# Optimization experiments

Hardware: AMD Instinct MI355X
Metric: run time of the kernel (lower is better)

Reference implementation:

```python
import jax, jax.numpy as jnp
import numpy as np

N_NODES = 4096
IN_FEAT = 256
N_HEADS = 8
N_HIDDEN = 64  # out_features // n_heads
NEG_SLOPE = 0.2
EDGE_PROB = 0.05


def setup_inputs() -> dict:
    key = jax.random.key(0)
    k1, k2, k3, k4 = jax.random.split(key, 4)
    h = jax.random.normal(k1, (N_NODES, IN_FEAT), dtype=jnp.float32)
    # binary adjacency mask [N, N, 1] (broadcast over heads), as in the torch asserts
    adj_mat = (jax.random.uniform(k2, (N_NODES, N_NODES, 1)) < EDGE_PROB).astype(jnp.float32)
    # nn.Linear(in_features, n_heads*n_hidden, bias=False) weight: [H*F, in]
    W = jax.random.normal(k3, (N_HEADS * N_HIDDEN, IN_FEAT), dtype=jnp.float32) / np.sqrt(IN_FEAT)
    # nn.Linear(2*n_hidden, 1, bias=False) weight, flattened: [2*F]
    a = jax.random.normal(k4, (2 * N_HIDDEN,), dtype=jnp.float32) / np.sqrt(2 * N_HIDDEN)
    return {"h": h, "adj_mat": adj_mat, "W": W, "a": a}


def reference(h, adj_mat, W, a):
    n = h.shape[0]
    # g: [N, H, F]
    g = (h @ W.T).reshape(n, N_HEADS, N_HIDDEN)
    # attn(cat[g_i, g_j]) == a_l . g_i + a_r . g_j  (linear, no bias)
    a_l = a[:N_HIDDEN]
    a_r = a[N_HIDDEN:]
    el = jnp.einsum('ihf,f->ih', g, a_l)  # [N, H]
    er = jnp.einsum('jhf,f->jh', g, a_r)  # [N, H]
    e = jax.nn.leaky_relu(el[:, None, :] + er[None, :, :], NEG_SLOPE)  # [N, N, H]
    # note: original multiplies scores by adjacency (not masked_fill)
    e = e * adj_mat  # adj broadcasts over heads
    att = jax.nn.softmax(e, axis=1)  # softmax over source nodes j
    # dropout is identity at eval (dropout_rate=0.0)
    out = jnp.einsum('ijh,jhf->ihf', att, g)  # [N, H, F]
    return out.reshape(n, N_HEADS * N_HIDDEN)
```

## Files before the change

kernel.cpp:

```cpp
#include <hip/hip_runtime.h>
#include <float.h>

#define N_NODES 4096
#define IN_FEAT 256
#define N_HEADS 8
#define N_HIDDEN 64
#define OUT_FEAT (N_HEADS * N_HIDDEN)
#define MAXE 512
#define NEG_SLOPE 0.2f

typedef _Float16 half8 __attribute__((ext_vector_type(8)));
typedef float floatx4 __attribute__((ext_vector_type(4)));
typedef float float8v __attribute__((ext_vector_type(8)));

__device__ inline unsigned fkey(float f) {
  unsigned u = __float_as_uint(f);
  return (u & 0x80000000u) ? ~u : (u | 0x80000000u);
}
__device__ inline float fkey_inv(unsigned k) {
  unsigned u = (k & 0x80000000u) ? (k & 0x7fffffffu) : ~k;
  return __uint_as_float(u);
}

__global__ __launch_bounds__(256) void gemm_fused(
    const float* __restrict__ H, const float* __restrict__ Wt,
    const float* __restrict__ a,
    _Float16* __restrict__ G16, float* __restrict__ el, float* __restrict__ er,
    float* __restrict__ gsum, unsigned* __restrict__ ermax_keys) {
  __shared__ _Float16 Ah[64][72], Al[64][72];
  __shared__ _Float16 Bh[64][72], Bl[64][72];
  const int t = threadIdx.x;
  const int w = t >> 6, l = t & 63;
  const int n16 = l & 15, q = l >> 4;
  const int bi = blockIdx.x, bo = blockIdx.y;
  const int m0 = bi * 64 + w * 16;

  floatx4 acc[4];
#pragma unroll
  for (int ct = 0; ct < 4; ++ct) acc[ct] = (floatx4)0.f;

  for (int kc = 0; kc < 4; ++kc) {
    if (kc) __syncthreads();
#pragma unroll
    for (int p = 0; p < 4; ++p) {
      const int idx = p * 256 + t;
      const int r = idx >> 4;
      const int c4 = (idx & 15) * 4;
      float4 hv = *(const float4*)(H + (size_t)(bi * 64 + r) * IN_FEAT + kc * 64 + c4);
      float4 wv = *(const float4*)(Wt + (size_t)(bo * 64 + r) * IN_FEAT + kc * 64 + c4);
      union { _Float16 h[4]; int2 d; } hh_, hl_, wh_, wl_;
      hh_.h[0] = (_Float16)hv.x; hh_.h[1] = (_Float16)hv.y;
      hh_.h[2] = (_Float16)hv.z; hh_.h[3] = (_Float16)hv.w;
      hl_.h[0] = (_Float16)(hv.x - (float)hh_.h[0]);
      hl_.h[1] = (_Float16)(hv.y - (float)hh_.h[1]);
      hl_.h[2] = (_Float16)(hv.z - (float)hh_.h[2]);
      hl_.h[3] = (_Float16)(hv.w - (float)hh_.h[3]);
      wh_.h[0] = (_Float16)wv.x; wh_.h[1] = (_Float16)wv.y;
      wh_.h[2] = (_Float16)wv.z; wh_.h[3] = (_Float16)wv.w;
      wl_.h[0] = (_Float16)(wv.x - (float)wh_.h[0]);
      wl_.h[1] = (_Float16)(wv.y - (float)wh_.h[1]);
      wl_.h[2] = (_Float16)(wv.z - (float)wh_.h[2]);
      wl_.h[3] = (_Float16)(wv.w - (float)wh_.h[3]);
      *(int2*)&Ah[r][c4] = hh_.d;
      *(int2*)&Al[r][c4] = hl_.d;
      *(int2*)&Bh[r][c4] = wh_.d;
      *(int2*)&Bl[r][c4] = wl_.d;
    }
    __syncthreads();
#pragma unroll
    for (int ks = 0; ks < 2; ++ks) {
      half8 Afh = *(const half8*)&Ah[w * 16 + n16][ks * 32 + q * 8];
      half8 Afl = *(const half8*)&Al[w * 16 + n16][ks * 32 + q * 8];
#pragma unroll
      for (int ct = 0; ct < 4; ++ct) {
        half8 Bfh = *(const half8*)&Bh[ct * 16 + n16][ks * 32 + q * 8];
        half8 Bfl = *(const half8*)&Bl[ct * 16 + n16][ks * 32 + q * 8];
        acc[ct] = __builtin_amdgcn_mfma_f32_16x16x32_f16(Afh, Bfh, acc[ct], 0, 0, 0);
        acc[ct] = __builtin_amdgcn_mfma_f32_16x16x32_f16(Afl, Bfh, acc[ct], 0, 0, 0);
        acc[ct] = __builtin_amdgcn_mfma_f32_16x16x32_f16(Afh, Bfl, acc[ct], 0, 0, 0);
      }
    }
  }

  float aLv[4], aRv[4];
#pragma unroll
  for (int ct = 0; ct < 4; ++ct) {
    aLv[ct] = a[ct * 16 + n16];
    aRv[ct] = a[64 + ct * 16 + n16];
  }

  float erv[4];
#pragma unroll
  for (int reg = 0; reg < 4; ++reg) {
    float sl = 0.f, sr = 0.f;
#pragma unroll
    for (int ct = 0; ct < 4; ++ct) {
      sl = fmaf(acc[ct][reg], aLv[ct], sl);
      sr = fmaf(acc[ct][reg], aRv[ct], sr);
    }
#pragma unroll
    for (int off = 1; off < 16; off <<= 1) {
      sl += __shfl_xor(sl, off);
      sr += __shfl_xor(sr, off);
    }
    erv[reg] = sr;
    if (n16 == 0) {
      const int rowi = m0 + q * 4 + reg;
      el[(size_t)rowi * N_HEADS + bo] = sl;
      er[(size_t)rowi * N_HEADS + bo] = sr;
    }
  }

  {
    float mx = fmaxf(fmaxf(erv[0], erv[1]), fmaxf(erv[2], erv[3]));
    mx = fmaxf(mx, __shfl_xor(mx, 16));
    mx = fmaxf(mx, __shfl_xor(mx, 32));
    if (l == 0) atomicMax(ermax_keys + bo, fkey(mx));
  }

#pragma unroll
  for (int ct = 0; ct < 4; ++ct) {
    float s = acc[ct][0] + acc[ct][1] + acc[ct][2] + acc[ct][3];
    s += __shfl_xor(s, 16);
    s += __shfl_xor(s, 32);
    if (l < 16) atomicAdd(gsum + bo * 64 + ct * 16 + n16, s);
  }

#pragma unroll
  for (int ct = 0; ct < 4; ++ct)
#pragma unroll
    for (int reg = 0; reg < 4; ++reg)
      G16[(size_t)(m0 + q * 4 + reg) * OUT_FEAT + bo * 64 + ct * 16 + n16] =
          (_Float16)acc[ct][reg];
}

__global__ __launch_bounds__(256, 8) void attn_sparse(
    const float* __restrict__ adj, const _Float16* __restrict__ G16,
    const float* __restrict__ el, const float* __restrict__ er,
    const unsigned* __restrict__ ermax_keys, const float* __restrict__ gsum,
    float* __restrict__ out) {
  __shared__ int jlist[MAXE];
  __shared__ _Float16 w16[MAXE * N_HEADS];
  __shared__ float accp[4][OUT_FEAT];
  __shared__ float el_s[N_HEADS], ermax_s[N_HEADS];
  __shared__ float zw[4][N_HEADS];
  __shared__ float em_s[N_HEADS], invz_s[N_HEADS];
  __shared__ int cnt;

  const int i = blockIdx.x;
  const int t = threadIdx.x;
  if (t == 0) cnt = 0;
  if (t < N_HEADS) {
    el_s[t] = el[(size_t)i * N_HEADS + t];
    ermax_s[t] = fkey_inv(ermax_keys[t]);
  }
  __syncthreads();

  const float* row = adj + (size_t)i * N_NODES;
#pragma unroll
  for (int q = 0; q < 4; ++q) {
    int j0 = (q * 256 + t) * 4;
    float4 v = *(const float4*)(row + j0);
    if (v.x != 0.f) { int p = atomicAdd(&cnt, 1); if (p < MAXE) jlist[p] = j0; }
    if (v.y != 0.f) { int p = atomicAdd(&cnt, 1); if (p < MAXE) jlist[p] = j0 + 1; }
    if (v.z != 0.f) { int p = atomicAdd(&cnt, 1); if (p < MAXE) jlist[p] = j0 + 2; }
    if (v.w != 0.f) { int p = atomicAdd(&cnt, 1); if (p < MAXE) jlist[p] = j0 + 3; }
  }
  __syncthreads();
  const int deg = min(cnt, MAXE);

  const int h2 = t & 7;
  const float m_h = fmaxf(0.f, el_s[h2] + ermax_s[h2]);
  const float em_h = __expf(-m_h);
  float zacc = 0.f;
  for (int jj = t >> 3; jj < deg; jj += 32) {
    int j = jlist[jj];
    float x = el_s[h2] + er[(size_t)j * N_HEADS + h2];
    x = fmaxf(x, NEG_SLOPE * x);
    float wv = __expf(x - m_h);
    zacc += wv;
    w16[jj * N_HEADS + h2] = (_Float16)wv;
  }
#pragma unroll
  for (int off = 8; off < 64; off <<= 1) zacc += __shfl_xor(zacc, off);
  if ((t & 63) < 8) zw[t >> 6][t & 7] = zacc;
  __syncthreads();
  if (t < 8) {
    float Z = zw[0][t] + zw[1][t] + zw[2][t] + zw[3][t] +
              (float)(N_NODES - deg) * em_h;
    invz_s[t] = 1.f / Z;
    em_s[t] = em_h;
  }

  const int wv4 = t >> 6;
  const int hh = (t >> 3) & 7;
  const int lq = t & 7;
  const float m_hh = fmaxf(0.f, el_s[hh] + ermax_s[hh]);
  const float em = __expf(-m_hh);
  float8v accv = (float8v)0.f;

  if (deg > 0) {
    const int last = deg - 1;
    const int e0 = wv4, e1 = wv4 + 4;
    float c0 = 0.f, c1 = 0.f;
    half8 g0, g1;
    {
      int ja = jlist[min(e0, last)];
      int jb = jlist[min(e1, last)];
      if (e0 < deg) c0 = (float)w16[e0 * N_HEADS + hh] - em;
      if (e1 < deg) c1 = (float)w16[e1 * N_HEADS + hh] - em;
      g0 = *(const half8*)(G16 + (size_t)ja * OUT_FEAT + hh * 64 + lq * 8);
      g1 = *(const half8*)(G16 + (size_t)jb * OUT_FEAT + hh * 64 + lq * 8);
    }
    for (int base = 0; base < deg; base += 8) {
      float cn0 = 0.f, cn1 = 0.f;
      half8 gn0 = g0, gn1 = g1;
      if (base + 8 < deg) {
        const int n0 = base + 8 + wv4, n1 = base + 12 + wv4;
        int ja = jlist[min(n0, last)];
        int jb = jlist[min(n1, last)];
        if (n0 < deg) cn0 = (float)w16[n0 * N_HEADS + hh] - em;
        if (n1 < deg) cn1 = (float)w16[n1 * N_HEADS + hh] - em;
        gn0 = *(const half8*)(G16 + (size_t)ja * OUT_FEAT + hh * 64 + lq * 8);
        gn1 = *(const half8*)(G16 + (size_t)jb * OUT_FEAT + hh * 64 + lq * 8);
      }
      accv += (float8v)c0 * __builtin_convertvector(g0, float8v);
      accv += (float8v)c1 * __builtin_convertvector(g1, float8v);
      c0 = cn0; g0 = gn0; c1 = cn1; g1 = gn1;
    }
  }
  {
    float4 a0 = make_float4(accv[0], accv[1], accv[2], accv[3]);
    float4 a1 = make_float4(accv[4], accv[5], accv[6], accv[7]);
    *(float4*)&accp[wv4][hh * 64 + lq * 8] = a0;
    *(float4*)&accp[wv4][hh * 64 + lq * 8 + 4] = a1;
  }
  __syncthreads();

  {
    const int c0 = t * 2;
    const int hf = c0 >> 6;
    float2 s = make_float2(0.f, 0.f);
#pragma unroll
    for (int g = 0; g < 4; ++g) {
      float2 p = *(const float2*)&accp[g][c0];
      s.x += p.x; s.y += p.y;
    }
    float2 gs = *(const float2*)(gsum + c0);
    const float emf = em_s[hf], iz = invz_s[hf];
    float2 o = make_float2((s.x + emf * gs.x) * iz, (s.y + emf * gs.y) * iz);
    *(float2*)(out + (size_t)i * OUT_FEAT + c0) = o;
  }
}

extern "C" void kernel_launch(void* const* d_in, const int* in_sizes, int n_in,
                              void* d_out, int out_size, void* d_ws, size_t ws_size,
                              hipStream_t stream) {
  const float* h   = (const float*)d_in[0];
  const float* adj = (const float*)d_in[1];
  const float* W   = (const float*)d_in[2];
  const float* a   = (const float*)d_in[3];
  float* out = (float*)d_out;

  char* ws = (char*)d_ws;
  _Float16* G16        = (_Float16*)ws;
  float*    el         = (float*)(ws + 4u * 1024 * 1024);
  float*    er         = (float*)(ws + 4u * 1024 * 1024 + 128 * 1024);
  float*    gsum       = (float*)(ws + 4u * 1024 * 1024 + 256 * 1024);
  unsigned* ermax_keys = (unsigned*)(ws + 4u * 1024 * 1024 + 258 * 1024);

  hipMemsetAsync(gsum, 0, 2048 + 32, stream);
  gemm_fused<<<dim3(64, 8), 256, 0, stream>>>(h, W, a, G16, el, er, gsum, ermax_keys);
  attn_sparse<<<dim3(N_NODES), 256, 0, stream>>>(adj, G16, el, er, ermax_keys, gsum, out);
}
```

Before: 179.8 us.

## Swizzle GEMM LDS with larger K chunk, stage G16 stores, use fdot2 aggregation

The GEMM now loads K in two 128-wide chunks into XOR-swizzled LDS tiles instead of four padded 64-wide chunks, with a launch-bounds occupancy hint. Its fp16 output is staged through LDS so each thread writes 16-byte coalesced rows. The sparse attention inner loop now computes weight coefficients in fp16 and accumulates with packed fdot2 instructions instead of converting G to float and using FMAs. The goals are fewer barriers, fewer bank conflicts and cheaper global stores and conversions. The cost is more LDS per block and lower coefficient precision, since the subtraction is now done in fp16.

```diff
diff --git a/kernel.cpp b/kernel.cpp
--- a/kernel.cpp
+++ b/kernel.cpp
@@ -8,10 +8,11 @@
 #define OUT_FEAT (N_HEADS * N_HIDDEN)
 #define MAXE 512
 #define NEG_SLOPE 0.2f
+#define KC 128
 
 typedef _Float16 half8 __attribute__((ext_vector_type(8)));
+typedef _Float16 half2v __attribute__((ext_vector_type(2)));
 typedef float floatx4 __attribute__((ext_vector_type(4)));
-typedef float float8v __attribute__((ext_vector_type(8)));
 
 __device__ inline unsigned fkey(float f) {
   unsigned u = __float_as_uint(f);
@@ -22,13 +23,15 @@
   return __uint_as_float(u);
 }
 
-__global__ __launch_bounds__(256) void gemm_fused(
+__global__ __launch_bounds__(256, 2) void gemm_fused(
     const float* __restrict__ H, const float* __restrict__ Wt,
     const float* __restrict__ a,
     _Float16* __restrict__ G16, float* __restrict__ el, float* __restrict__ er,
     float* __restrict__ gsum, unsigned* __restrict__ ermax_keys) {
-  __shared__ _Float16 Ah[64][72], Al[64][72];
-  __shared__ _Float16 Bh[64][72], Bl[64][72];
+  __shared__ _Float16 Ah[64 * KC];
+  __shared__ _Float16 Al[64 * KC];
+  __shared__ _Float16 Bh[64 * KC];
+  __shared__ _Float16 Bl[64 * KC];
   const int t = threadIdx.x;
   const int w = t >> 6, l = t & 63;
   const int n16 = l & 15, q = l >> 4;
@@ -39,15 +42,16 @@
 #pragma unroll
   for (int ct = 0; ct < 4; ++ct) acc[ct] = (floatx4)0.f;
 
-  for (int kc = 0; kc < 4; ++kc) {
+  for (int kc = 0; kc < 2; ++kc) {
     if (kc) __syncthreads();
 #pragma unroll
-    for (int p = 0; p < 4; ++p) {
+    for (int p = 0; p < 8; ++p) {
       const int idx = p * 256 + t;
-      const int r = idx >> 4;
-      const int c4 = (idx & 15) * 4;
-      float4 hv = *(const float4*)(H + (size_t)(bi * 64 + r) * IN_FEAT + kc * 64 + c4);
-      float4 wv = *(const float4*)(Wt + (size_t)(bo * 64 + r) * IN_FEAT + kc * 64 + c4);
+      const int r = idx >> 5;
+      const int c4 = (idx & 31) << 2;
+      const int dst = r * KC + (((idx & 31) >> 1) ^ (r & 7)) * 8 + (idx & 1) * 4;
+      float4 hv = *(const float4*)(H + (size_t)(bi * 64 + r) * IN_FEAT + kc * KC + c4);
+      float4 wv = *(const float4*)(Wt + (size_t)(bo * 64 + r) * IN_FEAT + kc * KC + c4);
       union { _Float16 h[4]; int2 d; } hh_, hl_, wh_, wl_;
       hh_.h[0] = (_Float16)hv.x; hh_.h[1] = (_Float16)hv.y;
       hh_.h[2] = (_Float16)hv.z; hh_.h[3] = (_Float16)hv.w;
@@ -61,20 +65,22 @@
       wl_.h[1] = (_Float16)(wv.y - (float)wh_.h[1]);
       wl_.h[2] = (_Float16)(wv.z - (float)wh_.h[2]);
       wl_.h[3] = (_Float16)(wv.w - (float)wh_.h[3]);
-      *(int2*)&Ah[r][c4] = hh_.d;
-      *(int2*)&Al[r][c4] = hl_.d;
-      *(int2*)&Bh[r][c4] = wh_.d;
-      *(int2*)&Bl[r][c4] = wl_.d;
+      *(int2*)&Ah[dst] = hh_.d;
+      *(int2*)&Al[dst] = hl_.d;
+      *(int2*)&Bh[dst] = wh_.d;
+      *(int2*)&Bl[dst] = wl_.d;
     }
     __syncthreads();
 #pragma unroll
-    for (int ks = 0; ks < 2; ++ks) {
-      half8 Afh = *(const half8*)&Ah[w * 16 + n16][ks * 32 + q * 8];
-      half8 Afl = *(const half8*)&Al[w * 16 + n16][ks * 32 + q * 8];
+    for (int ks = 0; ks < 4; ++ks) {
+      const int aoff = (w * 16 + n16) * KC + (((ks << 2) + q) ^ (n16 & 7)) * 8;
+      half8 Afh = *(const half8*)&Ah[aoff];
+      half8 Afl = *(const half8*)&Al[aoff];
 #pragma unroll
       for (int ct = 0; ct < 4; ++ct) {
-        half8 Bfh = *(const half8*)&Bh[ct * 16 + n16][ks * 32 + q * 8];
-        half8 Bfl = *(const half8*)&Bl[ct * 16 + n16][ks * 32 + q * 8];
+        const int boff = (ct * 16 + n16) * KC + (((ks << 2) + q) ^ (n16 & 7)) * 8;
+        half8 Bfh = *(const half8*)&Bh[boff];
+        half8 Bfl = *(const half8*)&Bl[boff];
         acc[ct] = __builtin_amdgcn_mfma_f32_16x16x32_f16(Afh, Bfh, acc[ct], 0, 0, 0);
         acc[ct] = __builtin_amdgcn_mfma_f32_16x16x32_f16(Afl, Bfh, acc[ct], 0, 0, 0);
         acc[ct] = __builtin_amdgcn_mfma_f32_16x16x32_f16(Afh, Bfl, acc[ct], 0, 0, 0);
@@ -126,12 +132,22 @@
     if (l < 16) atomicAdd(gsum + bo * 64 + ct * 16 + n16, s);
   }
 
+  __syncthreads();
+  _Float16* LG = Ah;
 #pragma unroll
   for (int ct = 0; ct < 4; ++ct)
 #pragma unroll
     for (int reg = 0; reg < 4; ++reg)
-      G16[(size_t)(m0 + q * 4 + reg) * OUT_FEAT + bo * 64 + ct * 16 + n16] =
-          (_Float16)acc[ct][reg];
+      LG[(w * 16 + q * 4 + reg) * 72 + ct * 16 + n16] = (_Float16)acc[ct][reg];
+  __syncthreads();
+  {
+    const int row = t >> 2, ch = t & 3;
+    int4 v0 = *(const int4*)&LG[row * 72 + ch * 16];
+    int4 v1 = *(const int4*)&LG[row * 72 + ch * 16 + 8];
+    _Float16* dst = G16 + (size_t)(bi * 64 + row) * OUT_FEAT + bo * 64 + ch * 16;
+    *(int4*)dst = v0;
+    *(int4*)(dst + 8) = v1;
+  }
 }
 
 __global__ __launch_bounds__(256, 8) void attn_sparse(
@@ -197,41 +213,63 @@
   const int lq = t & 7;
   const float m_hh = fmaxf(0.f, el_s[hh] + ermax_s[hh]);
   const float em = __expf(-m_hh);
-  float8v accv = (float8v)0.f;
+  const _Float16 em16 = (_Float16)em;
+  float accf[8];
+#pragma unroll
+  for (int k = 0; k < 8; ++k) accf[k] = 0.f;
 
   if (deg > 0) {
     const int last = deg - 1;
-    const int e0 = wv4, e1 = wv4 + 4;
-    float c0 = 0.f, c1 = 0.f;
+    _Float16 c0 = (_Float16)0.f, c1 = (_Float16)0.f;
     half8 g0, g1;
     {
+      const int e0 = wv4, e1 = wv4 + 4;
       int ja = jlist[min(e0, last)];
       int jb = jlist[min(e1, last)];
-      if (e0 < deg) c0 = (float)w16[e0 * N_HEADS + hh] - em;
-      if (e1 < deg) c1 = (float)w16[e1 * N_HEADS + hh] - em;
+      if (e0 < deg) c0 = w16[e0 * N_HEADS + hh] - em16;
+      if (e1 < deg) c1 = w16[e1 * N_HEADS + hh] - em16;
       g0 = *(const half8*)(G16 + (size_t)ja * OUT_FEAT + hh * 64 + lq * 8);
       g1 = *(const half8*)(G16 + (size_t)jb * OUT_FEAT + hh * 64 + lq * 8);
     }
     for (int base = 0; base < deg; base += 8) {
-      float cn0 = 0.f, cn1 = 0.f;
+      _Float16 cn0 = (_Float16)0.f, cn1 = (_Float16)0.f;
       half8 gn0 = g0, gn1 = g1;
       if (base + 8 < deg) {
         const int n0 = base + 8 + wv4, n1 = base + 12 + wv4;
         int ja = jlist[min(n0, last)];
         int jb = jlist[min(n1, last)];
-        if (n0 < deg) cn0 = (float)w16[n0 * N_HEADS + hh] - em;
-        if (n1 < deg) cn1 = (float)w16[n1 * N_HEADS + hh] - em;
+        if (n0 < deg) cn0 = w16[n0 * N_HEADS + hh] - em16;
+        if (n1 < deg) cn1 = w16[n1 * N_HEADS + hh] - em16;
         gn0 = *(const half8*)(G16 + (size_t)ja * OUT_FEAT + hh * 64 + lq * 8);
         gn1 = *(const half8*)(G16 + (size_t)jb * OUT_FEAT + hh * 64 + lq * 8);
       }
-      accv += (float8v)c0 * __builtin_convertvector(g0, float8v);
-      accv += (float8v)c1 * __builtin_convertvector(g1, float8v);
-      c0 = cn0; g0 = gn0; c1 = cn1; g1 = gn1;
+#if __has_builtin(__builtin_amdgcn_fdot2)
+      {
+        half2v c2 = {c0, c1};
+#pragma unroll
+        for (int d = 0; d < 4; ++d) {
+          half2v blo = {g0[2 * d], g1[2 * d]};
+          half2v bhi = {g0[2 * d + 1], g1[2 * d + 1]};
+          accf[2 * d] = __builtin_amdgcn_fdot2(c2, blo, accf[2 * d], false);
+          accf[2 * d + 1] = __builtin_amdgcn_fdot2(c2, bhi, accf[2 * d + 1], false);
+        }
+      }
+#else
+      {
+        const float f0 = (float)c0, f1 = (float)c1;
+#pragma unroll
+        for (int k = 0; k < 8; ++k) {
+          accf[k] = fmaf(f0, (float)g0[k], accf[k]);
+          accf[k] = fmaf(f1, (float)g1[k], accf[k]);
+        }
+      }
+#endif
+      c0 = cn0; c1 = cn1; g0 = gn0; g1 = gn1;
     }
   }
   {
-    float4 a0 = make_float4(accv[0], accv[1], accv[2], accv[3]);
-    float4 a1 = make_float4(accv[4], accv[5], accv[6], accv[7]);
+    float4 a0 = make_float4(accf[0], accf[1], accf[2], accf[3]);
+    float4 a1 = make_float4(accf[4], accf[5], accf[6], accf[7]);
     *(float4*)&accp[wv4][hh * 64 + lq * 8] = a0;
     *(float4*)&accp[wv4][hh * 64 + lq * 8 + 4] = a1;
   }
```

Result: faster. 174.3 us (-3.1%).
